# Kernel optimization log

Hardware: AMD Instinct MI355X
Metric: run time of the kernel (lower is better)

The kernel has to match this reference:

```python
import jax, jax.numpy as jnp
import numpy as np

B, S, E, H = 4, 2048, 1024, 16
DH = E // H  # head_dim = 64


def setup_inputs() -> dict:
    key = jax.random.key(0)
    k1, k2, k3 = jax.random.split(key, 3)
    x = jax.random.normal(k1, (B, S, E), dtype=jnp.float32)
    # xavier-uniform-like scale for dense kernels
    Wqkv = jax.random.normal(k2, (E, 3 * E), dtype=jnp.float32) * (1.0 / np.sqrt(E))
    Wout = jax.random.normal(k3, (E, E), dtype=jnp.float32) * (1.0 / np.sqrt(E))
    return {"x": x, "Wqkv": Wqkv, "Wout": Wout}


def reference(x, Wqkv, Wout):
    b, s, e = x.shape
    qkv = jnp.einsum("bse,ef->bsf", x, Wqkv)            # [B,S,3E]
    qkv = qkv.reshape(b, s, H, 3 * DH).transpose(0, 2, 1, 3)  # [B,H,S,3*DH]
    q, k, v = jnp.split(qkv, 3, axis=-1)                # each [B,H,S,DH]
    scale = 1.0 / jnp.sqrt(jnp.asarray(DH, dtype=x.dtype))
    scores = jnp.einsum("bhqd,bhkd->bhqk", q, k) * scale  # [B,H,S,S] materialized
    attn = jax.nn.softmax(scores, axis=-1)
    values = jnp.einsum("bhqk,bhkd->bhqd", attn, v)     # [B,H,S,DH]
    values = values.transpose(0, 2, 1, 3).reshape(b, s, e)
    out = jnp.einsum("bse,ef->bsf", values, Wout)       # [B,S,E]
    return out
```

## Files before the change

kernel.cpp:

```cpp
#include <hip/hip_runtime.h>

typedef __attribute__((ext_vector_type(8))) __bf16 bf16x8;
typedef __attribute__((ext_vector_type(4))) float f32x4;

#define LOG2E 1.4426950408889634f
#define QSCALE (0.125f * LOG2E)
#define SMAX_FIXED 13.0f

static __device__ __forceinline__ void gl_lds16(const void* g, void* l) {
  __builtin_amdgcn_global_load_lds(
      (__attribute__((address_space(1))) void*)(g),
      (__attribute__((address_space(3))) void*)(l), 16, 0, 0);
}

__global__ __launch_bounds__(256) void convert_f32_bf16(const float* __restrict__ in,
                                                        __bf16* __restrict__ out,
                                                        int n8) {
  const int i = blockIdx.x * 256 + threadIdx.x;
  if (i >= n8) return;
  const f32x4 a = *(const f32x4*)(in + (size_t)i * 8);
  const f32x4 b = *(const f32x4*)(in + (size_t)i * 8 + 4);
  bf16x8 o;
#pragma unroll
  for (int j = 0; j < 4; ++j) o[j] = (__bf16)a[j];
#pragma unroll
  for (int j = 0; j < 4; ++j) o[4 + j] = (__bf16)b[j];
  *(bf16x8*)(out + (size_t)i * 8) = o;
}

__global__ __launch_bounds__(256) void transpose_f32_bf16(
    const float* __restrict__ in, __bf16* __restrict__ out, int R, int C) {
  __shared__ __bf16 tile[64][72];
  const int t = threadIdx.x;
  const int c0 = blockIdx.x * 64;
  const int r0 = blockIdx.y * 64;
  const int lr = t >> 2;
  const int lc = (t & 3) * 16;
  const float* src = in + (size_t)(r0 + lr) * C + c0 + lc;
  bf16x8 w0, w1;
#pragma unroll
  for (int j = 0; j < 2; ++j) {
    const f32x4 a = *(const f32x4*)(src + j * 8);
    const f32x4 b = *(const f32x4*)(src + j * 8 + 4);
    bf16x8 o;
#pragma unroll
    for (int k = 0; k < 4; ++k) o[k] = (__bf16)a[k];
#pragma unroll
    for (int k = 0; k < 4; ++k) o[4 + k] = (__bf16)b[k];
    *(bf16x8*)&tile[lr][lc + j * 8] = o;
  }
  __syncthreads();
#pragma unroll
  for (int j = 0; j < 8; ++j) {
    w0[j] = tile[lc + j][lr];
    w1[j] = tile[lc + 8 + j][lr];
  }
  __bf16* dst = out + (size_t)(c0 + lr) * R + r0 + lc;
  *(bf16x8*)dst = w0;
  *(bf16x8*)(dst + 8) = w1;
}

template <int EPI>
__global__ __launch_bounds__(256) void gemm_bt(
    const __bf16* __restrict__ A, const __bf16* __restrict__ Bt,
    float* __restrict__ Cf, __bf16* __restrict__ q_ws, __bf16* __restrict__ k_ws,
    __bf16* __restrict__ vT_ws, int M, int N, int K) {
  __shared__ __bf16 sA[128 * 32];
  __shared__ __bf16 sB[128 * 32];
  const int t = threadIdx.x;
  const int lane = t & 63;
  const int w = t >> 6;
  const int quad = lane >> 4;
  const int l15 = lane & 15;
  const int wy = w >> 1, wx = w & 1;
  const int m0 = blockIdx.x * 128;
  const int n0 = blockIdx.y * 128;

  const f32x4 fzero = {0.f, 0.f, 0.f, 0.f};
  f32x4 acc[4][4];
#pragma unroll
  for (int i = 0; i < 4; ++i)
#pragma unroll
    for (int j = 0; j < 4; ++j) acc[i][j] = fzero;

  const int srow = t >> 2;
  const int scol = (t & 3) * 8;
  const __bf16* Ag = A + (size_t)(m0 + srow) * K + scol;
  const __bf16* Bg = Bt + (size_t)(n0 + srow) * K + scol;

  for (int k0 = 0; k0 < K; k0 += 32) {
    gl_lds16(Ag + k0, &sA[t * 8]);
    gl_lds16(Ag + (size_t)64 * K + k0, &sA[2048 + t * 8]);
    gl_lds16(Bg + k0, &sB[t * 8]);
    gl_lds16(Bg + (size_t)64 * K + k0, &sB[2048 + t * 8]);
    __syncthreads();
    bf16x8 af[4], bfr[4];
#pragma unroll
    for (int i = 0; i < 4; ++i)
      af[i] = *(const bf16x8*)&sA[(wy * 64 + i * 16 + l15) * 32 + quad * 8];
#pragma unroll
    for (int i = 0; i < 4; ++i)
      bfr[i] = *(const bf16x8*)&sB[(wx * 64 + i * 16 + l15) * 32 + quad * 8];
#pragma unroll
    for (int mi = 0; mi < 4; ++mi)
#pragma unroll
      for (int ni = 0; ni < 4; ++ni)
        acc[mi][ni] = __builtin_amdgcn_mfma_f32_16x16x32_bf16(af[mi], bfr[ni],
                                                              acc[mi][ni], 0, 0, 0);
    __syncthreads();
  }

#pragma unroll
  for (int mi = 0; mi < 4; ++mi) {
#pragma unroll
    for (int r = 0; r < 4; ++r) {
      const int row = m0 + wy * 64 + mi * 16 + quad * 4 + r;
#pragma unroll
      for (int ni = 0; ni < 4; ++ni) {
        const int col = n0 + wx * 64 + ni * 16 + l15;
        const float v = acc[mi][ni][r];
        if (EPI == 0) {
          const int b = row >> 11, s = row & 2047;
          const int h = col / 192;
          const int rr = col - h * 192;
          const int ty = rr >> 6, d = rr & 63;
          const int bh = b * 16 + h;
          if (ty == 0)
            q_ws[((size_t)bh * 2048 + s) * 64 + d] = (__bf16)v;
          else if (ty == 1)
            k_ws[((size_t)bh * 2048 + s) * 64 + d] = (__bf16)v;
          else
            vT_ws[((size_t)bh * 64 + d) * 2048 + s] = (__bf16)v;
        } else {
          Cf[(size_t)row * N + col] = v;
        }
      }
    }
  }
}

__global__ __launch_bounds__(256) void flash_attn(
    const __bf16* __restrict__ q_ws, const __bf16* __restrict__ k_ws,
    const __bf16* __restrict__ vT_ws, __bf16* __restrict__ values) {
  __shared__ __bf16 sK[64][72];
  __shared__ __bf16 sVt[64][72];
  __shared__ __bf16 sP[4][32][72];
  const int t = threadIdx.x;
  const int lane = t & 63, w = t >> 6, quad = lane >> 4, l15 = lane & 15;
  const int qt = blockIdx.x;
  const int bh = blockIdx.y;
  const __bf16* Qb = q_ws + (size_t)bh * 2048 * 64;
  const __bf16* Kb = k_ws + (size_t)bh * 2048 * 64;
  const __bf16* Vtb = vT_ws + (size_t)bh * 64 * 2048;
  const int qrow0 = qt * 128 + w * 32;

  bf16x8 qf[2][2];
#pragma unroll
  for (int mi = 0; mi < 2; ++mi)
#pragma unroll
    for (int ks = 0; ks < 2; ++ks)
      qf[mi][ks] = *(const bf16x8*)(Qb + (size_t)(qrow0 + mi * 16 + l15) * 64 +
                                    ks * 32 + quad * 8);

  bf16x8 ones;
#pragma unroll
  for (int j = 0; j < 8; ++j) ones[j] = (__bf16)1.0f;

  const f32x4 fzero = {0.f, 0.f, 0.f, 0.f};
  f32x4 accO[2][4];
  f32x4 accL[2];
#pragma unroll
  for (int mi = 0; mi < 2; ++mi) {
    accL[mi] = fzero;
#pragma unroll
    for (int ni = 0; ni < 4; ++ni) accO[mi][ni] = fzero;
  }

  const int srow = t >> 2;
  const int scol = (t & 3) * 16;

  bf16x8 ka, kb2, va, vb;
  {
    const __bf16* ks0 = Kb + (size_t)srow * 64 + scol;
    ka = *(const bf16x8*)ks0;
    kb2 = *(const bf16x8*)(ks0 + 8);
    const __bf16* vs0 = Vtb + (size_t)srow * 2048 + scol;
    va = *(const bf16x8*)vs0;
    vb = *(const bf16x8*)(vs0 + 8);
  }

  for (int kt = 0; kt < 32; ++kt) {
    *(bf16x8*)&sK[srow][scol] = ka;
    *(bf16x8*)&sK[srow][scol + 8] = kb2;
    *(bf16x8*)&sVt[srow][scol] = va;
    *(bf16x8*)&sVt[srow][scol + 8] = vb;
    __syncthreads();

    if (kt < 31) {
      const __bf16* ksn = Kb + (size_t)((kt + 1) * 64 + srow) * 64 + scol;
      ka = *(const bf16x8*)ksn;
      kb2 = *(const bf16x8*)(ksn + 8);
      const __bf16* vsn = Vtb + (size_t)srow * 2048 + (kt + 1) * 64 + scol;
      va = *(const bf16x8*)vsn;
      vb = *(const bf16x8*)(vsn + 8);
    }

    f32x4 accS[2][4];
#pragma unroll
    for (int mi = 0; mi < 2; ++mi)
#pragma unroll
      for (int ni = 0; ni < 4; ++ni) accS[mi][ni] = fzero;
#pragma unroll
    for (int ks = 0; ks < 2; ++ks) {
      bf16x8 kf[4];
#pragma unroll
      for (int ni = 0; ni < 4; ++ni)
        kf[ni] = *(const bf16x8*)&sK[ni * 16 + l15][ks * 32 + quad * 8];
#pragma unroll
      for (int mi = 0; mi < 2; ++mi)
#pragma unroll
        for (int ni = 0; ni < 4; ++ni)
          accS[mi][ni] = __builtin_amdgcn_mfma_f32_16x16x32_bf16(
              qf[mi][ks], kf[ni], accS[mi][ni], 0, 0, 0);
    }

#pragma unroll
    for (int mi = 0; mi < 2; ++mi) {
#pragma unroll
      for (int r = 0; r < 4; ++r) {
        const int prow = mi * 16 + quad * 4 + r;
#pragma unroll
        for (int ni = 0; ni < 4; ++ni) {
          const float p =
              __builtin_amdgcn_exp2f(accS[mi][ni][r] * QSCALE - SMAX_FIXED);
          sP[w][prow][ni * 16 + l15] = (__bf16)p;
        }
      }
    }
    __threadfence_block();

#pragma unroll
    for (int ks = 0; ks < 2; ++ks) {
      bf16x8 vf[4], pf[2];
#pragma unroll
      for (int ni = 0; ni < 4; ++ni)
        vf[ni] = *(const bf16x8*)&sVt[ni * 16 + l15][ks * 32 + quad * 8];
#pragma unroll
      for (int mi = 0; mi < 2; ++mi)
        pf[mi] = *(const bf16x8*)&sP[w][mi * 16 + l15][ks * 32 + quad * 8];
#pragma unroll
      for (int mi = 0; mi < 2; ++mi) {
#pragma unroll
        for (int ni = 0; ni < 4; ++ni)
          accO[mi][ni] = __builtin_amdgcn_mfma_f32_16x16x32_bf16(
              pf[mi], vf[ni], accO[mi][ni], 0, 0, 0);
        accL[mi] = __builtin_amdgcn_mfma_f32_16x16x32_bf16(pf[mi], ones, accL[mi],
                                                           0, 0, 0);
      }
    }
    __syncthreads();
  }

  const int b = bh >> 4, h = bh & 15;
#pragma unroll
  for (int mi = 0; mi < 2; ++mi) {
#pragma unroll
    for (int r = 0; r < 4; ++r) {
      const float inv = 1.0f / accL[mi][r];
      const int s = qrow0 + mi * 16 + quad * 4 + r;
#pragma unroll
      for (int ni = 0; ni < 4; ++ni)
        values[((size_t)(b * 2048 + s)) * 1024 + h * 64 + ni * 16 + l15] =
            (__bf16)(accO[mi][ni][r] * inv);
    }
  }
}

extern "C" void kernel_launch(void* const* d_in, const int* in_sizes, int n_in,
                              void* d_out, int out_size, void* d_ws, size_t ws_size,
                              hipStream_t stream) {
  (void)out_size; (void)ws_size;
  float* out = (float*)d_out;
  char* wsb = (char*)d_ws;
  __bf16* xb = (__bf16*)(wsb + 256);
  __bf16* WqkvT = xb + 8388608;
  __bf16* WoutT = WqkvT + 3145728;
  __bf16* q_ws = WoutT + 1048576;
  __bf16* k_ws = q_ws + 8388608;
  __bf16* vT_ws = k_ws + 8388608;
  __bf16* values = xb;

  const float *px = (const float*)d_in[0], *pw = (const float*)d_in[1],
              *po = (const float*)d_in[2];
  for (int i = 0; i < n_in; ++i) {
    if (in_sizes[i] == 8388608) px = (const float*)d_in[i];
    else if (in_sizes[i] == 3145728) pw = (const float*)d_in[i];
    else if (in_sizes[i] == 1048576) po = (const float*)d_in[i];
  }

  convert_f32_bf16<<<4096, 256, 0, stream>>>(px, xb, 1048576);
  transpose_f32_bf16<<<dim3(48, 16), 256, 0, stream>>>(pw, WqkvT, 1024, 3072);
  transpose_f32_bf16<<<dim3(16, 16), 256, 0, stream>>>(po, WoutT, 1024, 1024);
  gemm_bt<0><<<dim3(64, 24), 256, 0, stream>>>(xb, WqkvT, nullptr, q_ws, k_ws, vT_ws,
                                               8192, 3072, 1024);
  flash_attn<<<dim3(16, 64), 256, 0, stream>>>(q_ws, k_ws, vT_ws, values);
  gemm_bt<1><<<dim3(64, 8), 256, 0, stream>>>(values, WoutT, out, nullptr, nullptr,
                                              nullptr, 8192, 1024, 1024);
}
```

Before: 309.8 us.

## Replace 128x128 GEMM with 256x256 double-buffered pipelined GEMM kernel

Replaces the simple 128x128-tile GEMM, which loads one tile and then syncs, with a 256x256-tile, 512-thread kernel. The new kernel double-buffers 64-wide K slices in 128KB of dynamic LDS, swizzles the LDS layout to avoid bank conflicts, issues global-to-LDS loads between MFMA phases with explicit waitcnt and barriers, raises wave priority during MFMA bursts, and remaps block IDs for L2 locality. The aim is more data reuse per LDS load and overlap of memory traffic with matrix math. The risks are fewer blocks (384 and 128), which leaves the out-projection GEMM under-filling the GPU, plus high register pressure from the 8x4 accumulators.

New measurement: 314.7 us. Within noise of the previous version (+1.6%).

```diff
diff --git a/kernel.cpp b/kernel.cpp
--- a/kernel.cpp
+++ b/kernel.cpp
@@ -60,64 +60,163 @@
   *(bf16x8*)(dst + 8) = w1;
 }
 
+#define FENCEOFF
+
+#define STAGE_A(TT, KH)                                                  \
+  do {                                                                   \
+    const int kg_ = (TT) * 64 + (KH) * 32;                               \
+    char* d_ = lds + ((TT) & 1) * 32768 + (KH) * 16384 + t * 16;         \
+    gl_lds16(Ab + g0 + kg_, d_);                                         \
+    gl_lds16(Ab + g1 + kg_, d_ + 8192);                                  \
+  } while (0)
+
+#define STAGE_B(TT, KH)                                                  \
+  do {                                                                   \
+    const int kg_ = (TT) * 64 + (KH) * 32;                               \
+    char* d_ = lds + 65536 + ((TT) & 1) * 32768 + (KH) * 16384 + t * 16; \
+    gl_lds16(Bb + g0 + kg_, d_);                                         \
+    gl_lds16(Bb + g1 + kg_, d_ + 8192);                                  \
+  } while (0)
+
+#define READ_A(MIH, KK)                                                          \
+  do {                                                                           \
+    const char* p_ = lds + buf * 32768 + (KK) * 16384 +                          \
+                     (wm * 8 + (MIH) * 4) * 1024 + lfo;                          \
+    a0 = *(const bf16x8*)p_;                                                     \
+    a1 = *(const bf16x8*)(p_ + 1024);                                            \
+    a2 = *(const bf16x8*)(p_ + 2048);                                            \
+    a3 = *(const bf16x8*)(p_ + 3072);                                            \
+  } while (0)
+
+#define READ_B(KK)                                                               \
+  do {                                                                           \
+    const char* p_ = lds + 65536 + buf * 32768 + (KK) * 16384 + wn * 4096 + lfo; \
+    b0 = *(const bf16x8*)p_;                                                     \
+    b1 = *(const bf16x8*)(p_ + 1024);                                            \
+    b2 = *(const bf16x8*)(p_ + 2048);                                            \
+    b3 = *(const bf16x8*)(p_ + 3072);                                            \
+  } while (0)
+
+#define MROW(H, MI, AV)                                                          \
+  acc[(H) * 4 + (MI)][0] =                                                       \
+      __builtin_amdgcn_mfma_f32_16x16x32_bf16(AV, b0, acc[(H) * 4 + (MI)][0], 0, 0, 0); \
+  acc[(H) * 4 + (MI)][1] =                                                       \
+      __builtin_amdgcn_mfma_f32_16x16x32_bf16(AV, b1, acc[(H) * 4 + (MI)][1], 0, 0, 0); \
+  acc[(H) * 4 + (MI)][2] =                                                       \
+      __builtin_amdgcn_mfma_f32_16x16x32_bf16(AV, b2, acc[(H) * 4 + (MI)][2], 0, 0, 0); \
+  acc[(H) * 4 + (MI)][3] =                                                       \
+      __builtin_amdgcn_mfma_f32_16x16x32_bf16(AV, b3, acc[(H) * 4 + (MI)][3], 0, 0, 0);
+
+#define MFMA16(H)                      \
+  do {                                 \
+    __builtin_amdgcn_s_setprio(1);     \
+    MROW(H, 0, a0)                     \
+    MROW(H, 1, a1)                     \
+    MROW(H, 2, a2)                     \
+    MROW(H, 3, a3)                     \
+    __builtin_amdgcn_s_setprio(0);     \
+  } while (0)
+
 template <int EPI>
-__global__ __launch_bounds__(256) void gemm_bt(
+__global__ __launch_bounds__(512, 2) void gemm256(
     const __bf16* __restrict__ A, const __bf16* __restrict__ Bt,
     float* __restrict__ Cf, __bf16* __restrict__ q_ws, __bf16* __restrict__ k_ws,
     __bf16* __restrict__ vT_ws, int M, int N, int K) {
-  __shared__ __bf16 sA[128 * 32];
-  __shared__ __bf16 sB[128 * 32];
+  (void)M;
+  extern __shared__ char lds[];
   const int t = threadIdx.x;
   const int lane = t & 63;
+  const int quad = lane >> 4, l15 = lane & 15;
   const int w = t >> 6;
-  const int quad = lane >> 4;
-  const int l15 = lane & 15;
-  const int wy = w >> 1, wx = w & 1;
-  const int m0 = blockIdx.x * 128;
-  const int n0 = blockIdx.y * 128;
+  const int wm = w >> 2, wn = w & 3;
+
+  const int gx = gridDim.x;
+  int lid = blockIdx.y * gx + blockIdx.x;
+  lid = (lid & 7) * ((gx * gridDim.y) >> 3) + (lid >> 3);
+  const int m0 = (lid % gx) * 256;
+  const int n0 = (lid / gx) * 256;
+
+  int rowS[2], kcS[2];
+#pragma unroll
+  for (int l = 0; l < 2; ++l) {
+    const int LB = l * 8192 + t * 16;
+    const int r_in = (LB >> 6) & 15;
+    const int ch = ((LB >> 5) & 1) ^ ((r_in >> 3) & 1);
+    rowS[l] = (LB >> 10) * 16 + r_in;
+    kcS[l] = ch * 16 + ((LB >> 4) & 1) * 8;
+  }
+  const __bf16* Ab = A + (size_t)m0 * K;
+  const __bf16* Bb = Bt + (size_t)n0 * K;
+  const size_t g0 = (size_t)rowS[0] * K + kcS[0];
+  const size_t g1 = (size_t)rowS[1] * K + kcS[1];
+
+  const int lfo = l15 * 64 + ((((quad >> 1) ^ (l15 >> 3)) & 1) << 5) + ((quad & 1) << 4);
 
   const f32x4 fzero = {0.f, 0.f, 0.f, 0.f};
-  f32x4 acc[4][4];
-#pragma unroll
-  for (int i = 0; i < 4; ++i)
+  f32x4 acc[8][4];
+#pragma unroll
+  for (int i = 0; i < 8; ++i)
 #pragma unroll
     for (int j = 0; j < 4; ++j) acc[i][j] = fzero;
 
-  const int srow = t >> 2;
-  const int scol = (t & 3) * 8;
-  const __bf16* Ag = A + (size_t)(m0 + srow) * K + scol;
-  const __bf16* Bg = Bt + (size_t)(n0 + srow) * K + scol;
-
-  for (int k0 = 0; k0 < K; k0 += 32) {
-    gl_lds16(Ag + k0, &sA[t * 8]);
-    gl_lds16(Ag + (size_t)64 * K + k0, &sA[2048 + t * 8]);
-    gl_lds16(Bg + k0, &sB[t * 8]);
-    gl_lds16(Bg + (size_t)64 * K + k0, &sB[2048 + t * 8]);
-    __syncthreads();
-    bf16x8 af[4], bfr[4];
-#pragma unroll
-    for (int i = 0; i < 4; ++i)
-      af[i] = *(const bf16x8*)&sA[(wy * 64 + i * 16 + l15) * 32 + quad * 8];
-#pragma unroll
-    for (int i = 0; i < 4; ++i)
-      bfr[i] = *(const bf16x8*)&sB[(wx * 64 + i * 16 + l15) * 32 + quad * 8];
-#pragma unroll
-    for (int mi = 0; mi < 4; ++mi)
-#pragma unroll
-      for (int ni = 0; ni < 4; ++ni)
-        acc[mi][ni] = __builtin_amdgcn_mfma_f32_16x16x32_bf16(af[mi], bfr[ni],
-                                                              acc[mi][ni], 0, 0, 0);
-    __syncthreads();
-  }
-
-#pragma unroll
-  for (int mi = 0; mi < 4; ++mi) {
+  const int nt = K >> 6;
+  bf16x8 a0, a1, a2, a3, b0, b1, b2, b3;
+
+  STAGE_A(0, 0);
+  STAGE_B(0, 0);
+  STAGE_A(0, 1);
+  STAGE_B(0, 1);
+  if (nt > 1) {
+    STAGE_A(1, 0);
+    STAGE_B(1, 0);
+    asm volatile("s_waitcnt vmcnt(4)");
+  } else {
+    asm volatile("s_waitcnt vmcnt(0)");
+  }
+  __builtin_amdgcn_s_barrier();
+
+  for (int tt = 0; tt < nt; ++tt) {
+    const int buf = tt & 1;
+    READ_A(0, 0);
+    READ_B(0);
+    if (tt + 1 < nt) STAGE_A(tt + 1, 1);
+    __builtin_amdgcn_s_barrier();
+    asm volatile("s_waitcnt lgkmcnt(0)");
+    MFMA16(0);
+    __builtin_amdgcn_s_barrier();
+    READ_A(1, 0);
+    if (tt + 1 < nt) STAGE_B(tt + 1, 1);
+    __builtin_amdgcn_s_barrier();
+    asm volatile("s_waitcnt lgkmcnt(0)");
+    MFMA16(1);
+    __builtin_amdgcn_s_barrier();
+    READ_A(0, 1);
+    READ_B(1);
+    if (tt + 2 < nt) STAGE_A(tt + 2, 0);
+    __builtin_amdgcn_s_barrier();
+    asm volatile("s_waitcnt lgkmcnt(0)");
+    MFMA16(0);
+    __builtin_amdgcn_s_barrier();
+    READ_A(1, 1);
+    if (tt + 2 < nt) STAGE_B(tt + 2, 0);
+    __builtin_amdgcn_s_barrier();
+    asm volatile("s_waitcnt lgkmcnt(0)");
+    MFMA16(1);
+    if (tt + 2 < nt)
+      asm volatile("s_waitcnt vmcnt(4)");
+    else
+      asm volatile("s_waitcnt vmcnt(0)");
+    __builtin_amdgcn_s_barrier();
+  }
+
+#pragma unroll
+  for (int mi = 0; mi < 8; ++mi) {
 #pragma unroll
     for (int r = 0; r < 4; ++r) {
-      const int row = m0 + wy * 64 + mi * 16 + quad * 4 + r;
+      const int row = m0 + wm * 128 + mi * 16 + quad * 4 + r;
 #pragma unroll
       for (int ni = 0; ni < 4; ++ni) {
-        const int col = n0 + wx * 64 + ni * 16 + l15;
+        const int col = n0 + wn * 64 + ni * 16 + l15;
         const float v = acc[mi][ni][r];
         if (EPI == 0) {
           const int b = row >> 11, s = row & 2047;
@@ -298,12 +397,17 @@
     else if (in_sizes[i] == 1048576) po = (const float*)d_in[i];
   }
 
+  hipFuncSetAttribute(reinterpret_cast<const void*>(&gemm256<0>),
+                      hipFuncAttributeMaxDynamicSharedMemorySize, 131072);
+  hipFuncSetAttribute(reinterpret_cast<const void*>(&gemm256<1>),
+                      hipFuncAttributeMaxDynamicSharedMemorySize, 131072);
+
   convert_f32_bf16<<<4096, 256, 0, stream>>>(px, xb, 1048576);
   transpose_f32_bf16<<<dim3(48, 16), 256, 0, stream>>>(pw, WqkvT, 1024, 3072);
   transpose_f32_bf16<<<dim3(16, 16), 256, 0, stream>>>(po, WoutT, 1024, 1024);
-  gemm_bt<0><<<dim3(64, 24), 256, 0, stream>>>(xb, WqkvT, nullptr, q_ws, k_ws, vT_ws,
-                                               8192, 3072, 1024);
+  gemm256<0><<<dim3(32, 12), 512, 131072, stream>>>(xb, WqkvT, nullptr, q_ws, k_ws,
+                                                    vT_ws, 8192, 3072, 1024);
   flash_attn<<<dim3(16, 64), 256, 0, stream>>>(q_ws, k_ws, vT_ws, values);
-  gemm_bt<1><<<dim3(64, 8), 256, 0, stream>>>(values, WoutT, out, nullptr, nullptr,
-                                              nullptr, 8192, 1024, 1024);
-}
+  gemm256<1><<<dim3(32, 4), 512, 131072, stream>>>(values, WoutT, out, nullptr,
+                                                   nullptr, nullptr, 8192, 1024, 1024);
+}
```
